# Kernel tuning notes

Measured on AMD Instinct MI355X. Metric: run time of the kernel, lower is better.

The kernel has to match this reference:

```python
import jax, jax.numpy as jnp
import numpy as np

LN_EPS = 1e-5  # torch LayerNorm default


def _seg_mean(table, neigh_idx, num_seg):
    """Gather neighbor rows then unsorted-segment-mean (fixed fan-out S)."""
    S = neigh_idx.shape[0] // num_seg
    gathered = table[neigh_idx]  # [B*S, D] irregular gather
    seg = jnp.repeat(jnp.arange(num_seg), S)
    summed = jax.ops.segment_sum(gathered, seg, num_segments=num_seg)
    return summed / jnp.asarray(S, dtype=table.dtype)


def _block(agg, self_feats, W, b, gamma, beta):
    # concat -> Linear -> ReLU -> LayerNorm (dropout is identity in eval)
    h = jnp.concatenate([agg, self_feats], axis=-1) @ W + b
    h = jax.nn.relu(h)
    mu = jnp.mean(h, axis=-1, keepdims=True)
    var = jnp.mean((h - mu) ** 2, axis=-1, keepdims=True)
    return gamma * (h - mu) * jax.lax.rsqrt(var + LN_EPS) + beta


def setup_inputs() -> dict:
    key = jax.random.key(0)
    ks = jax.random.split(key, 10)
    N, D, H1, H2 = 100000, 256, 256, 256
    B, S1, S2 = 16384, 10, 10
    feats = jax.random.normal(ks[0], (N, D), dtype=jnp.float32)
    hidden1 = jax.random.uniform(ks[1], (N, H1), dtype=jnp.float32)  # torch.rand init
    hidden2 = jax.random.uniform(ks[2], (N, H2), dtype=jnp.float32)
    node_batch = jax.random.randint(ks[3], (B,), 0, N)
    neigh1 = jax.random.randint(ks[4], (B * S1,), 0, N)
    neigh2 = jax.random.randint(ks[5], (B * S2,), 0, N)
    W1 = jax.random.normal(ks[6], (2 * D, H1), dtype=jnp.float32) * 0.05
    W2 = jax.random.normal(ks[7], (2 * H1, H2), dtype=jnp.float32) * 0.05
    return {
        "feats": feats, "hidden1": hidden1, "hidden2": hidden2,
        "W1": W1, "b1": jnp.zeros((H1,)), "g1": jnp.ones((H1,)), "be1": jnp.zeros((H1,)),
        "W2": W2, "b2": jnp.zeros((H2,)), "g2": jnp.ones((H2,)), "be2": jnp.zeros((H2,)),
        "node_batch": node_batch, "neigh1": neigh1, "neigh2": neigh2,
    }


def reference(feats, hidden1, hidden2, W1, b1, g1, be1, W2, b2, g2, be2,
              node_batch, neigh1, neigh2):
    B = node_batch.shape[0]
    # layer 1: aggregate raw features (hidden['layer 0'])
    agg1 = _seg_mean(feats, neigh1, B)
    h1 = _block(agg1, feats[node_batch], W1, b1, g1, be1)  # [B, H1]
    # layer 2: aggregate from the OLD hidden1 table (original updates tables
    # only after the loop finishes)
    agg2 = _seg_mean(hidden1, neigh2, B)
    h2 = _block(agg2, hidden1[node_batch], W2, b2, g2, be2)  # [B, H2]
    new_hidden2 = hidden2.at[node_batch].set(h2)
    return h2, new_hidden2
```

## Files before the change

kernel.cpp:

```cpp
#include <hip/hip_runtime.h>

#define HDIM 256
#define KDIM 512
#define ROWS 16
#define XBPAD 8
#define LN_EPS 1e-5f
#define COPY_BLOCKS 1024

typedef __attribute__((ext_vector_type(8))) short bf16x8;
typedef __attribute__((ext_vector_type(4))) float f32x4;

static __device__ __forceinline__ unsigned short f2bf(float f) {
    union { float f; unsigned u; } v; v.f = f;
    unsigned r = v.u + 0x7FFF + ((v.u >> 16) & 1);
    return (unsigned short)(r >> 16);
}

__global__ __launch_bounds__(256) void prep_init_kernel(
    const float* __restrict__ W2, unsigned short* __restrict__ W2f,
    int* __restrict__ winner, const int* __restrict__ node_batch, int B)
{
    int tid = blockIdx.x * 256 + threadIdx.x;
    for (int i = tid; i < B; i += 64 * 256) winner[node_batch[i]] = -1;
    if (tid >= 16 * 16 * 64) return;
    int l  = tid & 63;
    int ks = (tid >> 6) & 15;
    int ct = tid >> 10;
    int col = ct * 16 + (l & 15);
    int k0  = ks * 32 + (l >> 4) * 8;
    unsigned short pk[8];
    #pragma unroll
    for (int j = 0; j < 8; ++j)
        pk[j] = f2bf(W2[(size_t)(k0 + j) * HDIM + col]);
    *(uint4*)&W2f[(size_t)tid * 8] = *(uint4*)pk;
}

template <int SC>
__global__ __launch_bounds__(512, 4) void fused_kernel(
    const float* __restrict__ hidden1,
    const f32x4* __restrict__ h2src,
    const unsigned short* __restrict__ W2f,
    const int* __restrict__ node_batch,
    const int* __restrict__ neigh2,
    int* __restrict__ winner,
    float* __restrict__ hout,
    float* __restrict__ out_tab,
    int n4, int B, int S_rt)
{
    if ((blockIdx.x & 1) == 0) {
        const int tid = (blockIdx.x >> 1) * 512 + threadIdx.x;
        const int stride = COPY_BLOCKS * 512;
        f32x4* dst = (f32x4*)out_tab;
        for (int i = tid; i < n4; i += stride) {
            f32x4 v = __builtin_nontemporal_load(&h2src[i]);
            __builtin_nontemporal_store(v, &dst[i]);
        }
        for (int i = tid; i < B; i += stride) atomicMax(&winner[node_batch[i]], i);
        return;
    }

    __shared__ unsigned short xbf[ROWS][KDIM + XBPAD];
    const int t    = threadIdx.x;
    const int lane = t & 63;
    const int w    = t >> 6;
    const int row0 = (blockIdx.x >> 1) * ROWS;

    #pragma unroll
    for (int rr = 0; rr < 2; ++rr) {
        const int r = w + rr * 8;
        int b = row0 + r;
        if (b >= B) b = B - 1;
        const int selfidx = node_batch[b];
        float4 a = make_float4(0.f, 0.f, 0.f, 0.f);
        if constexpr (SC > 0) {
            const int* nb = neigh2 + (size_t)b * SC;
            int idx[SC > 0 ? SC : 1];
            #pragma unroll
            for (int s = 0; s < SC; ++s) idx[s] = nb[s];
            #pragma unroll
            for (int s = 0; s < SC; ++s) {
                float4 v = *(const float4*)&hidden1[(size_t)idx[s] * HDIM + 4 * lane];
                a.x += v.x; a.y += v.y; a.z += v.z; a.w += v.w;
            }
            const float invS = 1.0f / (float)SC;
            a.x *= invS; a.y *= invS; a.z *= invS; a.w *= invS;
        } else {
            const int* nb = neigh2 + (size_t)b * S_rt;
            for (int s = 0; s < S_rt; ++s) {
                float4 v = *(const float4*)&hidden1[(size_t)nb[s] * HDIM + 4 * lane];
                a.x += v.x; a.y += v.y; a.z += v.z; a.w += v.w;
            }
            const float invS = 1.0f / (float)S_rt;
            a.x *= invS; a.y *= invS; a.z *= invS; a.w *= invS;
        }
        float4 sv = *(const float4*)&hidden1[(size_t)selfidx * HDIM + 4 * lane];
        unsigned short pa[4] = { f2bf(a.x), f2bf(a.y), f2bf(a.z), f2bf(a.w) };
        unsigned short ps[4] = { f2bf(sv.x), f2bf(sv.y), f2bf(sv.z), f2bf(sv.w) };
        *(uint2*)&xbf[r][4 * lane]        = *(uint2*)pa;
        *(uint2*)&xbf[r][HDIM + 4 * lane] = *(uint2*)ps;
    }
    __syncthreads();

    const int arow = lane & 15;
    const int g8   = (lane >> 4) * 8;
    f32x4 acc0 = {0.f, 0.f, 0.f, 0.f};
    f32x4 acc1 = {0.f, 0.f, 0.f, 0.f};
    const unsigned short* bp0 = W2f + ((size_t)(2 * w) * 1024 + lane) * 8;
    const unsigned short* bp1 = W2f + ((size_t)(2 * w + 1) * 1024 + lane) * 8;

    #pragma unroll
    for (int ks = 0; ks < 16; ++ks) {
        bf16x8 af = *(const bf16x8*)&xbf[arow][ks * 32 + g8];
        bf16x8 b0 = *(const bf16x8*)(bp0 + ks * 512);
        bf16x8 b1 = *(const bf16x8*)(bp1 + ks * 512);
        acc0 = __builtin_amdgcn_mfma_f32_16x16x32_bf16(af, b0, acc0, 0, 0, 0);
        acc1 = __builtin_amdgcn_mfma_f32_16x16x32_bf16(af, b1, acc1, 0, 0, 0);
    }

    #pragma unroll
    for (int p = 0; p < 4; ++p) {
        const int drow = (lane >> 4) * 4 + p;
        const size_t rbase = (size_t)(row0 + drow) * HDIM;
        hout[rbase + 2 * w * 16 + (lane & 15)]       = acc0[p];
        hout[rbase + (2 * w + 1) * 16 + (lane & 15)] = acc1[p];
    }
}

__global__ __launch_bounds__(512) void ln_kernel(
    float* __restrict__ out_h2,
    float* __restrict__ out_tab,
    const float* __restrict__ bias2,
    const float* __restrict__ gamma2,
    const float* __restrict__ beta2,
    const int* __restrict__ node_batch,
    const int* __restrict__ winner,
    int B)
{
    const int lane = threadIdx.x & 63;
    const int row  = blockIdx.x * 8 + (threadIdx.x >> 6);
    if (row >= B) return;

    float4 hv = *(const float4*)&out_h2[(size_t)row * HDIM + 4 * lane];
    float4 bb = *(const float4*)&bias2[4 * lane];
    float4 gg = *(const float4*)&gamma2[4 * lane];
    float4 ee = *(const float4*)&beta2[4 * lane];
    float bbar[4] = {bb.x, bb.y, bb.z, bb.w};
    float gar[4]  = {gg.x, gg.y, gg.z, gg.w};
    float ear[4]  = {ee.x, ee.y, ee.z, ee.w};

    float v[4];
    float s = 0.f, q = 0.f;
    {
        float hh[4] = {hv.x, hv.y, hv.z, hv.w};
        #pragma unroll
        for (int jj = 0; jj < 4; ++jj) {
            float h = fmaxf(hh[jj] + bbar[jj], 0.0f);
            v[jj] = h;
            s += h;
            q += h * h;
        }
    }
    #pragma unroll
    for (int off = 32; off > 0; off >>= 1) {
        s += __shfl_xor(s, off, 64);
        q += __shfl_xor(q, off, 64);
    }
    float mu   = s * (1.0f / (float)HDIM);
    float var  = q * (1.0f / (float)HDIM) - mu * mu;
    float rstd = rsqrtf(var + LN_EPS);

    f32x4 o;
    o[0] = gar[0] * (v[0] - mu) * rstd + ear[0];
    o[1] = gar[1] * (v[1] - mu) * rstd + ear[1];
    o[2] = gar[2] * (v[2] - mu) * rstd + ear[2];
    o[3] = gar[3] * (v[3] - mu) * rstd + ear[3];
    __builtin_nontemporal_store(o, (f32x4*)&out_h2[(size_t)row * HDIM + 4 * lane]);
    int node = node_batch[row];
    if (winner[node] == row)
        __builtin_nontemporal_store(o, (f32x4*)&out_tab[(size_t)node * HDIM + 4 * lane]);
}

extern "C" void kernel_launch(void* const* d_in, const int* in_sizes, int n_in,
                              void* d_out, int out_size, void* d_ws, size_t ws_size,
                              hipStream_t stream) {
    const float* hidden1 = (const float*)d_in[1];
    const float* hidden2 = (const float*)d_in[2];
    const float* W2      = (const float*)d_in[7];
    const float* b2      = (const float*)d_in[8];
    const float* g2      = (const float*)d_in[9];
    const float* be2     = (const float*)d_in[10];
    const int* node_batch = (const int*)d_in[11];
    const int* neigh2     = (const int*)d_in[13];

    const int B  = in_sizes[11];
    const int S  = in_sizes[13] / B;
    const int NH = in_sizes[2];

    float* out_h2  = (float*)d_out;
    float* out_tab = out_h2 + (size_t)B * HDIM;
    int* winner = (int*)d_ws;
    unsigned short* W2f = (unsigned short*)((char*)d_ws + 512 * 1024);

    hipLaunchKernelGGL(prep_init_kernel, dim3(64), dim3(256), 0, stream,
                       W2, W2f, winner, node_batch, B);

    const int mfma_blocks = (B + ROWS - 1) / ROWS;
    dim3 grid(2 * ((COPY_BLOCKS > mfma_blocks) ? COPY_BLOCKS : mfma_blocks));
    if (S == 10) {
        hipLaunchKernelGGL((fused_kernel<10>), grid, dim3(512), 0, stream,
                           hidden1, (const f32x4*)hidden2, W2f,
                           node_batch, neigh2, winner, out_h2, out_tab,
                           NH / 4, B, S);
    } else {
        hipLaunchKernelGGL((fused_kernel<0>), grid, dim3(512), 0, stream,
                           hidden1, (const f32x4*)hidden2, W2f,
                           node_batch, neigh2, winner, out_h2, out_tab,
                           NH / 4, B, S);
    }
    hipLaunchKernelGGL(ln_kernel, dim3((B + 7) / 8), dim3(512), 0, stream,
                       out_h2, out_tab, b2, g2, be2, node_batch, winner, B);
}
```

Measured before the change: 79.34 us.

## Split hidden2 table copy across fused and LayerNorm kernels, skip overwritten rows

The full-table copy of hidden2 into the output is split in half. The first half stays interleaved with the gather+MFMA kernel. The second half moves into the LayerNorm kernel, where one block in three copies while the other two normalize. Rows whose node already has a winner are skipped in the second half, since LayerNorm overwrites them. This balances bandwidth-bound copy work against both compute phases and adds an extra winner lookup per copied vector.

Measured after the change: 92.34 us. 16.4% more time.

```diff
diff --git a/kernel.cpp b/kernel.cpp
--- a/kernel.cpp
+++ b/kernel.cpp
@@ -45,13 +45,13 @@
     int* __restrict__ winner,
     float* __restrict__ hout,
     float* __restrict__ out_tab,
-    int n4, int B, int S_rt)
+    int half4, int B, int S_rt)
 {
     if ((blockIdx.x & 1) == 0) {
         const int tid = (blockIdx.x >> 1) * 512 + threadIdx.x;
         const int stride = COPY_BLOCKS * 512;
         f32x4* dst = (f32x4*)out_tab;
-        for (int i = tid; i < n4; i += stride) {
+        for (int i = tid; i < half4; i += stride) {
             f32x4 v = __builtin_nontemporal_load(&h2src[i]);
             __builtin_nontemporal_store(v, &dst[i]);
         }
@@ -126,21 +126,36 @@
     }
 }
 
-__global__ __launch_bounds__(512) void ln_kernel(
+__global__ __launch_bounds__(512) void ln_copy_kernel(
     float* __restrict__ out_h2,
     float* __restrict__ out_tab,
+    const f32x4* __restrict__ h2src,
     const float* __restrict__ bias2,
     const float* __restrict__ gamma2,
     const float* __restrict__ beta2,
     const int* __restrict__ node_batch,
     const int* __restrict__ winner,
-    int B)
+    int half4, int n4, int ncopy, int B)
 {
+    if (blockIdx.x % 3 == 0) {
+        const int tid = (blockIdx.x / 3) * 512 + threadIdx.x;
+        const int stride = ncopy * 512;
+        f32x4* dst = (f32x4*)out_tab;
+        for (int i = half4 + tid; i < n4; i += stride) {
+            if (winner[i >> 6] >= 0) continue;
+            f32x4 v = __builtin_nontemporal_load(&h2src[i]);
+            __builtin_nontemporal_store(v, &dst[i]);
+        }
+        return;
+    }
+
+    const int lnid = (blockIdx.x / 3) * 2 + (blockIdx.x % 3) - 1;
     const int lane = threadIdx.x & 63;
-    const int row  = blockIdx.x * 8 + (threadIdx.x >> 6);
+    const int row  = lnid * 8 + (threadIdx.x >> 6);
     if (row >= B) return;
 
-    float4 hv = *(const float4*)&out_h2[(size_t)row * HDIM + 4 * lane];
+    f32x4 hv = __builtin_nontemporal_load(
+        (const f32x4*)&out_h2[(size_t)row * HDIM + 4 * lane]);
     float4 bb = *(const float4*)&bias2[4 * lane];
     float4 gg = *(const float4*)&gamma2[4 * lane];
     float4 ee = *(const float4*)&beta2[4 * lane];
@@ -150,15 +165,12 @@
 
     float v[4];
     float s = 0.f, q = 0.f;
-    {
-        float hh[4] = {hv.x, hv.y, hv.z, hv.w};
-        #pragma unroll
-        for (int jj = 0; jj < 4; ++jj) {
-            float h = fmaxf(hh[jj] + bbar[jj], 0.0f);
-            v[jj] = h;
-            s += h;
-            q += h * h;
-        }
+    #pragma unroll
+    for (int jj = 0; jj < 4; ++jj) {
+        float h = fmaxf(hv[jj] + bbar[jj], 0.0f);
+        v[jj] = h;
+        s += h;
+        q += h * h;
     }
     #pragma unroll
     for (int off = 32; off > 0; off >>= 1) {
@@ -195,6 +207,8 @@
     const int B  = in_sizes[11];
     const int S  = in_sizes[13] / B;
     const int NH = in_sizes[2];
+    const int n4 = NH / 4;
+    const int half4 = n4 / 2;
 
     float* out_h2  = (float*)d_out;
     float* out_tab = out_h2 + (size_t)B * HDIM;
@@ -205,18 +219,24 @@
                        W2, W2f, winner, node_batch, B);
 
     const int mfma_blocks = (B + ROWS - 1) / ROWS;
-    dim3 grid(2 * ((COPY_BLOCKS > mfma_blocks) ? COPY_BLOCKS : mfma_blocks));
+    dim3 grid2(2 * ((COPY_BLOCKS > mfma_blocks) ? COPY_BLOCKS : mfma_blocks));
     if (S == 10) {
-        hipLaunchKernelGGL((fused_kernel<10>), grid, dim3(512), 0, stream,
+        hipLaunchKernelGGL((fused_kernel<10>), grid2, dim3(512), 0, stream,
                            hidden1, (const f32x4*)hidden2, W2f,
                            node_batch, neigh2, winner, out_h2, out_tab,
-                           NH / 4, B, S);
+                           half4, B, S);
     } else {
-        hipLaunchKernelGGL((fused_kernel<0>), grid, dim3(512), 0, stream,
+        hipLaunchKernelGGL((fused_kernel<0>), grid2, dim3(512), 0, stream,
                            hidden1, (const f32x4*)hidden2, W2f,
                            node_batch, neigh2, winner, out_h2, out_tab,
-                           NH / 4, B, S);
-    }
-    hipLaunchKernelGGL(ln_kernel, dim3((B + 7) / 8), dim3(512), 0, stream,
-                       out_h2, out_tab, b2, g2, be2, node_batch, winner, B);
-}
+                           half4, B, S);
+    }
+
+    const int nln   = (B + 7) / 8;
+    const int ncopy = (nln + 1) / 2;
+    dim3 grid3(3 * ncopy);
+    hipLaunchKernelGGL(ln_copy_kernel, grid3, dim3(512), 0, stream,
+                       out_h2, out_tab, (const f32x4*)hidden2,
+                       b2, g2, be2, node_batch, winner,
+                       half4, n4, ncopy, B);
+}
```
